# Kernel tuning notes

Hardware: AMD Instinct MI355X
Metric: run time of the kernel (lower is better)

## Reference

```python
import jax, jax.numpy as jnp
import numpy as np

N, F, D, E, L, T = 20000, 512, 256, 200000, 3, 2  # nodes, raw feat, hidden, edges/etype, layers, etypes


def _layernorm(x, g, b, eps=1e-5):
    mu = jnp.mean(x, axis=-1, keepdims=True)
    var = jnp.mean(jnp.square(x - mu), axis=-1, keepdims=True)
    return (x - mu) * jax.lax.rsqrt(var + eps) * g + b


def setup_inputs() -> dict:
    key = jax.random.key(0)
    ks = jax.random.split(key, 12)
    s = 0.02
    return {
        "x": jax.random.normal(ks[0], (N, F), dtype=jnp.float32),
        "src": jax.random.randint(ks[1], (T, E), 0, N, dtype=jnp.int32),
        "dst": jax.random.randint(ks[2], (T, E), 0, N, dtype=jnp.int32),
        # HeteroLinear (single ntype)
        "Wlin": jax.random.normal(ks[3], (D, F), dtype=jnp.float32) * s,
        "blin": jnp.zeros((D,), dtype=jnp.float32),
        # stacked per-layer, per-etype SAGEConv('pool') params
        "Wpool": jax.random.normal(ks[4], (L, T, D, D), dtype=jnp.float32) * s,
        "bpool": jnp.zeros((L, T, D), dtype=jnp.float32),
        "Wself": jax.random.normal(ks[5], (L, T, D, D), dtype=jnp.float32) * s,
        "Wneigh": jax.random.normal(ks[6], (L, T, D, D), dtype=jnp.float32) * s,
        "bconv": jnp.zeros((L, T, D), dtype=jnp.float32),
        "gamma": jnp.ones((L, T, D), dtype=jnp.float32),
        "beta": jnp.zeros((L, T, D), dtype=jnp.float32),
    }


def reference(x, src, dst, Wlin, blin, Wpool, bpool, Wself, Wneigh, bconv, gamma, beta):
    n = x.shape[0]
    # HeteroLinear: raw features -> embed
    h = x @ Wlin.T + blin
    for l in range(L):
        out = None
        for t in range(T):  # per edge-type SAGEConv, aggregator='pool'
            hp = jax.nn.relu(h @ Wpool[l, t].T + bpool[l, t])        # fc_pool + relu on src nodes
            m = hp[src[t]]                                            # gather [E, D]
            neigh = jax.ops.segment_max(m, dst[t], num_segments=n)    # max-pool reduce
            neigh = jnp.where(jnp.isneginf(neigh), 0.0, neigh)        # zero-in-degree -> 0 (DGL)
            rst = h @ Wself[l, t].T + neigh @ Wneigh[l, t].T + bconv[l, t]
            if l < L - 1:
                rst = jax.nn.relu(rst)                                # activation before norm
            rst = _layernorm(rst, gamma[l, t], beta[l, t])
            out = rst if out is None else out + rst                   # HeteroGraphConv 'sum'
        h = out
    return h
```

## Files before the change

kernel.cpp:

```cpp
#include <hip/hip_runtime.h>

#define N_NODES 20000
#define F_IN    512
#define D_H     256
#define E_EDGES 200000
#define L_LAYERS 3
#define T_ETYPES 2

typedef __attribute__((ext_vector_type(8))) short bf16x8;
typedef __attribute__((ext_vector_type(4))) float f32x4;

__device__ __forceinline__ unsigned short f2b(float f) {
    unsigned int u = __float_as_uint(f);
    u = (u + 0x7FFFu + ((u >> 16) & 1u)) >> 16;
    return (unsigned short)u;
}
__device__ __forceinline__ unsigned int pack2(float a, float b) {
    return (unsigned int)f2b(a) | ((unsigned int)f2b(b) << 16);
}

__device__ __forceinline__ void gload16(const unsigned short* g, unsigned short* l)
{
    __builtin_amdgcn_global_load_lds(
        (const __attribute__((address_space(1))) void*)g,
        (__attribute__((address_space(3))) void*)l, 16, 0, 0);
}

__device__ __forceinline__ void shufg8(const float* __restrict__ s,
                                       unsigned short* __restrict__ d,
                                       int NO, int K, int o8)
{
    const int matsz8 = (NO * K) >> 3;
    const int mat = o8 / matsz8;
    const int rem = o8 - mat * matsz8;
    const int dst = rem << 3;
    const int slab = dst >> 12;
    const int w = dst & 4095;
    const int spr = K >> 5;
    const int slab_n = slab / spr, slab_k = slab - slab_n * spr;
    const int nl = (((w >> 9) & 7) << 4) + ((w >> 3) & 15);
    const int kk = ((w >> 7) & 3) << 3;
    const size_t soff = (size_t)mat * NO * K + (size_t)(slab_n * 128 + nl) * K
                      + slab_k * 32 + kk;
    const float4 a = *(const float4*)(s + soff);
    const float4 b = *(const float4*)(s + soff + 4);
    uint4 u;
    u.x = pack2(a.x, a.y); u.y = pack2(a.z, a.w);
    u.z = pack2(b.x, b.y); u.w = pack2(b.z, b.w);
    *(uint4*)(d + (size_t)mat * NO * K + dst) = u;
}

__global__ __launch_bounds__(256) void prep_kernel(
    const float* __restrict__ x,  unsigned short* __restrict__ xb, int nx8,
    const float* __restrict__ s0, unsigned short* __restrict__ d0, int NO0, int K0, int n08,
    const float* __restrict__ s1, unsigned short* __restrict__ d1, int NO1, int K1, int n18,
    const float* __restrict__ s2, unsigned short* __restrict__ d2, int NO2, int K2, int n28,
    const float* __restrict__ s3, unsigned short* __restrict__ d3, int NO3, int K3, int n38)
{
    int i = blockIdx.x * 256 + threadIdx.x;
    if (i < nx8) {
        const float4 a = ((const float4*)x)[i * 2];
        const float4 b = ((const float4*)x)[i * 2 + 1];
        uint4 u;
        u.x = pack2(a.x, a.y); u.y = pack2(a.z, a.w);
        u.z = pack2(b.x, b.y); u.w = pack2(b.z, b.w);
        ((uint4*)xb)[i] = u;
        return;
    }
    i -= nx8;
    if (i < n08) { shufg8(s0, d0, NO0, K0, i); return; }
    if ((i -= n08) < n18) { shufg8(s1, d1, NO1, K1, i); return; }
    if ((i -= n18) < n28) { shufg8(s2, d2, NO2, K2, i); return; }
    if ((i -= n28) < n38) { shufg8(s3, d3, NO3, K3, i); return; }
}

template <int NSTEPS>
__global__ __launch_bounds__(256) void gemm_lds(
    const unsigned short* __restrict__ A,
    const unsigned short* __restrict__ Wf,
    const float* __restrict__ bias, unsigned short* __restrict__ Cout,
    int M, int ldc, int relu)
{
    __shared__ __align__(16) unsigned short As[3][4096];
    __shared__ __align__(16) unsigned short Bs[3][4096];
    const int K = NSTEPS * 32;
    const int tid = threadIdx.x, lane = tid & 63, w = tid >> 6;
    const int wm = w >> 1, wn = w & 1;
    const int bm = blockIdx.y * 128, bn = blockIdx.x * 128;
    const unsigned short* slab0 = Wf + (((size_t)blockIdx.x * NSTEPS) << 12);

    size_t aoff[2];
#pragma unroll
    for (int q = 0; q < 2; ++q) {
        const int c = q * 256 + tid;
        const int mi = c >> 6, ww = c & 63, r = ww & 15, kq = ww >> 4;
        const int rg = min(bm + mi * 16 + r, M - 1);
        aoff[q] = (size_t)rg * K + kq * 8;
    }

    const int cbase = bn + wn * 64 + (lane & 15);
    float bj[4];
#pragma unroll
    for (int j = 0; j < 4; ++j) bj[j] = bias[cbase + j * 16];
    asm volatile("" ::: "memory");

    f32x4 acc[4][4] = {};

#define GL_STAGE(S, BUF) do { \
    _Pragma("unroll") \
    for (int q_ = 0; q_ < 2; ++q_) { \
        gload16(A + aoff[q_] + (S) * 32, &As[BUF][(q_ * 256 + w * 64) * 8]); \
        gload16(slab0 + (((size_t)(S)) << 12) + (size_t)(q_ * 256 + tid) * 8, \
                &Bs[BUF][(q_ * 256 + w * 64) * 8]); \
    } \
} while (0)

    GL_STAGE(0, 0);
    GL_STAGE(1, 1);
#pragma unroll
    for (int s = 0; s < NSTEPS; ++s) {
        if (s + 1 < NSTEPS) asm volatile("s_waitcnt vmcnt(4)" ::: "memory");
        else                asm volatile("s_waitcnt vmcnt(0)" ::: "memory");
        __builtin_amdgcn_s_barrier();
        asm volatile("" ::: "memory");
        if (s + 2 < NSTEPS) GL_STAGE(s + 2, (s + 2) % 3);
        const int buf = s % 3;
        bf16x8 a[4], b[4];
#pragma unroll
        for (int mi = 0; mi < 4; ++mi)
            a[mi] = *(const bf16x8*)((const char*)As[buf] + ((wm * 4 + mi) << 10) + lane * 16);
#pragma unroll
        for (int j = 0; j < 4; ++j)
            b[j] = *(const bf16x8*)((const char*)Bs[buf] + ((wn * 4 + j) << 10) + lane * 16);
#pragma unroll
        for (int mi = 0; mi < 4; ++mi)
#pragma unroll
            for (int j = 0; j < 4; ++j)
                acc[mi][j] = __builtin_amdgcn_mfma_f32_16x16x32_bf16(a[mi], b[j], acc[mi][j], 0, 0, 0);
    }
#undef GL_STAGE

    const int rb = bm + wm * 64 + ((lane >> 4) << 2);
#pragma unroll
    for (int j = 0; j < 4; ++j) {
#pragma unroll
        for (int mi = 0; mi < 4; ++mi)
#pragma unroll
            for (int r = 0; r < 4; ++r) {
                const int row = rb + mi * 16 + r;
                if (row < M) {
                    float v = acc[mi][j][r] + bj[j];
                    if (relu) v = fmaxf(v, 0.f);
                    Cout[(size_t)row * ldc + cbase + j * 16] = f2b(v);
                }
            }
    }
}

template <int RELU>
__global__ __launch_bounds__(256) void tail_gemm(
    const unsigned short* __restrict__ h,
    const unsigned short* __restrict__ neigh,
    const unsigned short* __restrict__ Ws,
    const unsigned short* __restrict__ Wn,
    const float* __restrict__ bias,
    float* __restrict__ R)
{
    __shared__ __align__(16) unsigned short As[3][4096];
    __shared__ __align__(16) unsigned short Bs[3][4096];
    const int tid = threadIdx.x, lane = tid & 63, w = tid >> 6;
    const int wm = w >> 1, wn = w & 1;
    const int bm = blockIdx.y * 128;
    const int cs = blockIdx.x;
    const int e  = cs >> 1;
    const unsigned short* Bself  = Ws + (size_t)e * 65536 + (cs & 1) * 32768;
    const unsigned short* Bneigh = Wn + (size_t)e * 65536 + (cs & 1) * 32768;

    size_t aoffH[2], aoffN[2];
#pragma unroll
    for (int q = 0; q < 2; ++q) {
        const int c = q * 256 + tid;
        const int mi = c >> 6, ww = c & 63, r = ww & 15, kq = ww >> 4;
        const int rg = min(bm + mi * 16 + r, N_NODES - 1);
        aoffH[q] = (size_t)rg * 256 + kq * 8;
        aoffN[q] = (size_t)rg * 512 + e * 256 + kq * 8;
    }

    const int cbase = cs * 128 + wn * 64 + (lane & 15);
    float bj[4];
#pragma unroll
    for (int j = 0; j < 4; ++j) bj[j] = bias[cbase + j * 16];
    asm volatile("" ::: "memory");

    f32x4 acc[4][4] = {};

#define TG_STAGE(S, BUF) do { \
    _Pragma("unroll") \
    for (int q_ = 0; q_ < 2; ++q_) { \
        const unsigned short* as_ = ((S) < 8) ? (h + aoffH[q_] + (S) * 32) \
                                              : (neigh + aoffN[q_] + ((S) - 8) * 32); \
        gload16(as_, &As[BUF][(q_ * 256 + w * 64) * 8]); \
        const unsigned short* bs_ = (((S) < 8) ? (Bself + (S) * 4096) \
                                               : (Bneigh + ((S) - 8) * 4096)) \
                                    + (size_t)(q_ * 256 + tid) * 8; \
        gload16(bs_, &Bs[BUF][(q_ * 256 + w * 64) * 8]); \
    } \
} while (0)

    TG_STAGE(0, 0);
    TG_STAGE(1, 1);
#pragma unroll
    for (int s = 0; s < 16; ++s) {
        if (s + 1 < 16) asm volatile("s_waitcnt vmcnt(4)" ::: "memory");
        else            asm volatile("s_waitcnt vmcnt(0)" ::: "memory");
        __builtin_amdgcn_s_barrier();
        asm volatile("" ::: "memory");
        if (s + 2 < 16) TG_STAGE(s + 2, (s + 2) % 3);
        const int buf = s % 3;
        bf16x8 a[4], b[4];
#pragma unroll
        for (int mi = 0; mi < 4; ++mi)
            a[mi] = *(const bf16x8*)((const char*)As[buf] + ((wm * 4 + mi) << 10) + lane * 16);
#pragma unroll
        for (int j = 0; j < 4; ++j)
            b[j] = *(const bf16x8*)((const char*)Bs[buf] + ((wn * 4 + j) << 10) + lane * 16);
#pragma unroll
        for (int mi = 0; mi < 4; ++mi)
#pragma unroll
            for (int j = 0; j < 4; ++j)
                acc[mi][j] = __builtin_amdgcn_mfma_f32_16x16x32_bf16(a[mi], b[j], acc[mi][j], 0, 0, 0);
    }
#undef TG_STAGE

    const int rb = bm + wm * 64 + ((lane >> 4) << 2);
#pragma unroll
    for (int j = 0; j < 4; ++j) {
#pragma unroll
        for (int mi = 0; mi < 4; ++mi)
#pragma unroll
            for (int r = 0; r < 4; ++r) {
                const int row = rb + mi * 16 + r;
                if (row < N_NODES) {
                    float v = acc[mi][j][r] + bj[j];
                    if (RELU) v = fmaxf(v, 0.f);
                    R[(size_t)row * 512 + cbase + j * 16] = v;
                }
            }
    }
}

template <int LAST>
__global__ __launch_bounds__(256) void ln_sum_kernel(
    const float* __restrict__ R,
    const float* __restrict__ gamma,
    const float* __restrict__ beta,
    void* __restrict__ outp)
{
    const int row  = blockIdx.x * 4 + (threadIdx.x >> 6);
    const int lane = threadIdx.x & 63;
    const float4 v0 = ((const float4*)R)[(size_t)row * 128 + lane];
    const float4 v1 = ((const float4*)R)[(size_t)row * 128 + 64 + lane];
    float s0 = v0.x + v0.y + v0.z + v0.w;
    float q0 = v0.x * v0.x + v0.y * v0.y + v0.z * v0.z + v0.w * v0.w;
    float s1 = v1.x + v1.y + v1.z + v1.w;
    float q1 = v1.x * v1.x + v1.y * v1.y + v1.z * v1.z + v1.w * v1.w;
#pragma unroll
    for (int o = 1; o < 64; o <<= 1) {
        s0 += __shfl_xor(s0, o); q0 += __shfl_xor(q0, o);
        s1 += __shfl_xor(s1, o); q1 += __shfl_xor(q1, o);
    }
    const float m0 = s0 * (1.f / 256.f), m1 = s1 * (1.f / 256.f);
    const float i0 = rsqrtf(q0 * (1.f / 256.f) - m0 * m0 + 1e-5f);
    const float i1 = rsqrtf(q1 * (1.f / 256.f) - m1 * m1 + 1e-5f);
    const float4 g0 = ((const float4*)gamma)[lane];
    const float4 b0 = ((const float4*)beta)[lane];
    const float4 g1 = ((const float4*)(gamma + 256))[lane];
    const float4 b1 = ((const float4*)(beta + 256))[lane];
    const float o0 = (v0.x - m0) * i0 * g0.x + b0.x + (v1.x - m1) * i1 * g1.x + b1.x;
    const float o1 = (v0.y - m0) * i0 * g0.y + b0.y + (v1.y - m1) * i1 * g1.y + b1.y;
    const float o2 = (v0.z - m0) * i0 * g0.z + b0.z + (v1.z - m1) * i1 * g1.z + b1.z;
    const float o3 = (v0.w - m0) * i0 * g0.w + b0.w + (v1.w - m1) * i1 * g1.w + b1.w;
    if (LAST) {
        ((float4*)outp)[(size_t)row * 64 + lane] = make_float4(o0, o1, o2, o3);
    } else {
        ushort4 u;
        u.x = f2b(o0); u.y = f2b(o1); u.z = f2b(o2); u.w = f2b(o3);
        ((ushort4*)outp)[(size_t)row * 64 + lane] = u;
    }
}

__global__ __launch_bounds__(256) void count_deg_kernel(
    const int* __restrict__ dst, int* __restrict__ cnt, int E2)
{
    int e = blockIdx.x * 256 + threadIdx.x;
    if (e < E2) {
        const int base = (e >= E_EDGES) ? N_NODES : 0;
        atomicAdd(&cnt[base + dst[e]], 1);
    }
}

__global__ __launch_bounds__(256) void scanA_kernel(
    const int* __restrict__ cnt, int* __restrict__ incl, int* __restrict__ bsum, int n)
{
    __shared__ int tmp[256];
    const int tid = threadIdx.x;
    const int i = blockIdx.x * 256 + tid;
    const int v = (i < n) ? cnt[i] : 0;
    tmp[tid] = v;
    __syncthreads();
#pragma unroll
    for (int o = 1; o < 256; o <<= 1) {
        const int t = (tid >= o) ? tmp[tid - o] : 0;
        __syncthreads();
        tmp[tid] += t;
        __syncthreads();
    }
    if (i < n) incl[i] = tmp[tid];
    if (tid == 255) bsum[blockIdx.x] = tmp[255];
}

__global__ __launch_bounds__(256) void scanB_kernel(int* __restrict__ bsum, int nb)
{
    __shared__ int tmp[256];
    const int tid = threadIdx.x;
    const int v = (tid < nb) ? bsum[tid] : 0;
    tmp[tid] = v;
    __syncthreads();
#pragma unroll
    for (int o = 1; o < 256; o <<= 1) {
        const int t = (tid >= o) ? tmp[tid - o] : 0;
        __syncthreads();
        tmp[tid] += t;
        __syncthreads();
    }
    if (tid < nb) bsum[tid] = tmp[tid] - v;
}

__global__ __launch_bounds__(256) void scanC_kernel(
    const int* __restrict__ cnt, const int* __restrict__ incl,
    const int* __restrict__ bsum, int* __restrict__ off, int* __restrict__ cursor, int n)
{
    const int i = blockIdx.x * 256 + threadIdx.x;
    if (i < n) {
        const int e = incl[i] + bsum[blockIdx.x];
        off[i + 1] = e;
        cursor[i] = e - cnt[i];
    }
    if (i == 0) off[0] = 0;
}

__global__ __launch_bounds__(256) void fill_csr_kernel(
    const int* __restrict__ src, const int* __restrict__ dst,
    int* __restrict__ cursor, int* __restrict__ esrc, int E2)
{
    int e = blockIdx.x * 256 + threadIdx.x;
    if (e < E2) {
        const int base = (e >= E_EDGES) ? N_NODES : 0;
        const int pos = atomicAdd(&cursor[base + dst[e]], 1);
        esrc[pos] = src[e];
    }
}

__device__ __forceinline__ ushort4 umax4(ushort4 a, ushort4 b)
{
    a.x = a.x > b.x ? a.x : b.x;
    a.y = a.y > b.y ? a.y : b.y;
    a.z = a.z > b.z ? a.z : b.z;
    a.w = a.w > b.w ? a.w : b.w;
    return a;
}

__global__ __launch_bounds__(256) void seg_max_kernel(
    const unsigned short* __restrict__ hp, const int* __restrict__ off,
    const int* __restrict__ esrc, unsigned short* __restrict__ neigh)
{
    const int g = blockIdx.x * 4 + (threadIdx.x >> 6);
    if (g >= 2 * N_NODES) return;
    const int t = (g >= N_NODES) ? 1 : 0;
    const int node = g - t * N_NODES;
    const int lane = threadIdx.x & 63;
    const int co = t * D_H + lane * 4;
    const int e0 = off[g], e1 = off[g + 1];
    ushort4 acc = make_ushort4(0, 0, 0, 0);
    int e = e0;
    for (; e + 4 <= e1; e += 4) {
        const int s0 = esrc[e + 0], s1 = esrc[e + 1];
        const int s2 = esrc[e + 2], s3 = esrc[e + 3];
        const ushort4 v0 = *(const ushort4*)(hp + (size_t)s0 * 512 + co);
        const ushort4 v1 = *(const ushort4*)(hp + (size_t)s1 * 512 + co);
        const ushort4 v2 = *(const ushort4*)(hp + (size_t)s2 * 512 + co);
        const ushort4 v3 = *(const ushort4*)(hp + (size_t)s3 * 512 + co);
        acc = umax4(umax4(umax4(acc, v0), umax4(v1, v2)), v3);
    }
    for (; e < e1; ++e)
        acc = umax4(acc, *(const ushort4*)(hp + (size_t)esrc[e] * 512 + co));
    *(ushort4*)(neigh + (size_t)node * 512 + co) = acc;
}

extern "C" void kernel_launch(void* const* d_in, const int* in_sizes, int n_in,
                              void* d_out, int out_size, void* d_ws, size_t ws_size,
                              hipStream_t stream)
{
    const float* x      = (const float*)d_in[0];
    const int*   src    = (const int*)d_in[1];
    const int*   dst    = (const int*)d_in[2];
    const float* Wlin   = (const float*)d_in[3];
    const float* blin   = (const float*)d_in[4];
    const float* Wpool  = (const float*)d_in[5];
    const float* bpool  = (const float*)d_in[6];
    const float* Wself  = (const float*)d_in[7];
    const float* Wneigh = (const float*)d_in[8];
    const float* bconv  = (const float*)d_in[9];
    const float* gamma  = (const float*)d_in[10];
    const float* beta   = (const float*)d_in[11];

    const size_t NB = (size_t)N_NODES * D_H;
    char* p = (char*)d_ws;
    unsigned short* hp_b    = (unsigned short*)p; p += NB * 2 * T_ETYPES;
    unsigned short* neigh_b = (unsigned short*)p; p += NB * 2 * T_ETYPES;
    unsigned short* h_a     = (unsigned short*)p; p += NB * 2;
    unsigned short* h_b     = (unsigned short*)p; p += NB * 2;
    unsigned short* xb      = (unsigned short*)p; p += (size_t)N_NODES * F_IN * 2;
    float*          Rbuf    = (float*)p;          p += (size_t)N_NODES * 512 * 4;
    unsigned short* wlin_f  = (unsigned short*)p; p += (size_t)D_H * F_IN * 2;
    const size_t WSZ = (size_t)L_LAYERS * T_ETYPES * D_H * D_H;
    unsigned short* wpool_f = (unsigned short*)p; p += WSZ * 2;
    unsigned short* wself_f = (unsigned short*)p; p += WSZ * 2;
    unsigned short* wneigh_f= (unsigned short*)p; p += WSZ * 2;
    int* ip = (int*)p;
    const int NT = T_ETYPES * N_NODES;
    int* cnt    = ip; ip += NT;
    int* incl   = ip; ip += NT;
    int* off    = ip; ip += NT + 1;
    int* cursor = ip; ip += NT;
    int* esrc   = ip; ip += T_ETYPES * E_EDGES;
    int* bsum   = ip; ip += 256;

    const dim3 blk(256);
    const int E2 = T_ETYPES * E_EDGES;
    const dim3 e2grid((E2 + 255) / 256);
    const int nScanBlk = (NT + 255) / 256;

    {
        const int nx8  = N_NODES * F_IN / 8;
        const int nl8  = D_H * F_IN / 8;
        const int nw8  = (int)(WSZ / 8);
        const int tot  = nx8 + nl8 + 3 * nw8;
        prep_kernel<<<dim3((tot + 255) / 256), blk, 0, stream>>>(
            x, xb, nx8,
            Wlin, wlin_f, D_H, F_IN, nl8,
            Wpool, wpool_f, T_ETYPES * D_H, D_H, nw8,
            Wself, wself_f, D_H, D_H, nw8,
            Wneigh, wneigh_f, D_H, D_H, nw8);
    }

    hipMemsetAsync(cnt, 0, (size_t)NT * sizeof(int), stream);
    count_deg_kernel<<<e2grid, blk, 0, stream>>>(dst, cnt, E2);
    scanA_kernel<<<dim3(nScanBlk), blk, 0, stream>>>(cnt, incl, bsum, NT);
    scanB_kernel<<<dim3(1), blk, 0, stream>>>(bsum, nScanBlk);
    scanC_kernel<<<dim3(nScanBlk), blk, 0, stream>>>(cnt, incl, bsum, off, cursor, NT);
    fill_csr_kernel<<<e2grid, blk, 0, stream>>>(src, dst, cursor, esrc, E2);

    const int MB = (N_NODES + 127) / 128;

    gemm_lds<16><<<dim3(2, MB), blk, 0, stream>>>(
        xb, wlin_f, blin, h_a, N_NODES, D_H, 0);

    unsigned short* h = h_a;
    unsigned short* hn = h_b;
    const dim3 sgrid((2 * N_NODES + 3) / 4);
    const dim3 lngrid(N_NODES / 4);
    for (int l = 0; l < L_LAYERS; ++l) {
        gemm_lds<8><<<dim3(4, MB), blk, 0, stream>>>(
            h, wpool_f + (size_t)l * T_ETYPES * D_H * D_H,
            bpool + (size_t)l * T_ETYPES * D_H, hp_b, N_NODES, T_ETYPES * D_H, 1);
        seg_max_kernel<<<sgrid, blk, 0, stream>>>(hp_b, off, esrc, neigh_b);
        const size_t wlo = (size_t)l * T_ETYPES * D_H * D_H;
        const size_t blo = (size_t)l * T_ETYPES * D_H;
        if (l < L_LAYERS - 1) {
            tail_gemm<1><<<dim3(4, MB), blk, 0, stream>>>(
                h, neigh_b, wself_f + wlo, wneigh_f + wlo, bconv + blo, Rbuf);
            ln_sum_kernel<0><<<lngrid, blk, 0, stream>>>(
                Rbuf, gamma + blo, beta + blo, hn);
        } else {
            tail_gemm<0><<<dim3(4, MB), blk, 0, stream>>>(
                h, neigh_b, wself_f + wlo, wneigh_f + wlo, bconv + blo, Rbuf);
            ln_sum_kernel<1><<<lngrid, blk, 0, stream>>>(
                Rbuf, gamma + blo, beta + blo, d_out);
        }
        unsigned short* tmp = h; h = hn; hn = tmp;
    }
}
```

Measured before the change: 410.2 us.

## Use 512-thread GEMM blocks with 4x2 wave split and grouped block ordering

Both GEMM kernels move from 256-thread blocks, where each wave computes a 64x64 tile, to 512-thread blocks, where each wave computes a 64x32 tile. Each thread now issues one A and one B async load per stage instead of two, so the vmcnt wait drops from 4 to 2. The 2D grid becomes a 1D grid that walks groups of 8 row-blocks across all column slabs, so neighbouring blocks share the A rows in L2. Accumulators per thread are halved, which may allow more waves in flight, at the cost of more blocks and barriers spanning 8 waves.

```diff
diff --git a/kernel.cpp b/kernel.cpp
--- a/kernel.cpp
+++ b/kernel.cpp
@@ -74,8 +74,8 @@
     if ((i -= n28) < n38) { shufg8(s3, d3, NO3, K3, i); return; }
 }
 
-template <int NSTEPS>
-__global__ __launch_bounds__(256) void gemm_lds(
+template <int NSTEPS, int CS>
+__global__ __launch_bounds__(512) void gemm_lds(
     const unsigned short* __restrict__ A,
     const unsigned short* __restrict__ Wf,
     const float* __restrict__ bias, unsigned short* __restrict__ Cout,
@@ -84,65 +84,61 @@
     __shared__ __align__(16) unsigned short As[3][4096];
     __shared__ __align__(16) unsigned short Bs[3][4096];
     const int K = NSTEPS * 32;
-    const int tid = threadIdx.x, lane = tid & 63, w = tid >> 6;
-    const int wm = w >> 1, wn = w & 1;
-    const int bm = blockIdx.y * 128, bn = blockIdx.x * 128;
-    const unsigned short* slab0 = Wf + (((size_t)blockIdx.x * NSTEPS) << 12);
-
-    size_t aoff[2];
-#pragma unroll
-    for (int q = 0; q < 2; ++q) {
-        const int c = q * 256 + tid;
-        const int mi = c >> 6, ww = c & 63, r = ww & 15, kq = ww >> 4;
-        const int rg = min(bm + mi * 16 + r, M - 1);
-        aoff[q] = (size_t)rg * K + kq * 8;
-    }
-
-    const int cbase = bn + wn * 64 + (lane & 15);
-    float bj[4];
-#pragma unroll
-    for (int j = 0; j < 4; ++j) bj[j] = bias[cbase + j * 16];
+    const int tid = threadIdx.x, lane = tid & 63;
+    const int w = tid >> 6, wm = w >> 2, wn = w & 3;
+    const int id = blockIdx.x;
+    const int g = id / (8 * CS), rem = id - g * (8 * CS);
+    const int cs = rem >> 3, bmi = (g << 3) | (rem & 7);
+    const int MB = (M + 127) >> 7;
+    if (bmi >= MB) return;
+    const int bm = bmi * 128;
+    const unsigned short* slab0 = Wf + (((size_t)cs * NSTEPS) << 12);
+
+    const int rg = min(bm + ((tid >> 6) << 4) + (tid & 15), M - 1);
+    const size_t aoff = (size_t)rg * K + ((tid >> 4) & 3) * 8;
+    const unsigned short* bsrc = slab0 + (size_t)tid * 8;
+
+    const int cbase = cs * 128 + wn * 32 + (lane & 15);
+    float bj[2];
+#pragma unroll
+    for (int j = 0; j < 2; ++j) bj[j] = bias[cbase + j * 16];
     asm volatile("" ::: "memory");
 
-    f32x4 acc[4][4] = {};
+    f32x4 acc[4][2] = {};
 
 #define GL_STAGE(S, BUF) do { \
-    _Pragma("unroll") \
-    for (int q_ = 0; q_ < 2; ++q_) { \
-        gload16(A + aoff[q_] + (S) * 32, &As[BUF][(q_ * 256 + w * 64) * 8]); \
-        gload16(slab0 + (((size_t)(S)) << 12) + (size_t)(q_ * 256 + tid) * 8, \
-                &Bs[BUF][(q_ * 256 + w * 64) * 8]); \
-    } \
+    gload16(A + aoff + (S) * 32, &As[BUF][(size_t)tid * 8]); \
+    gload16(bsrc + (((size_t)(S)) << 12), &Bs[BUF][(size_t)tid * 8]); \
 } while (0)
 
     GL_STAGE(0, 0);
     GL_STAGE(1, 1);
 #pragma unroll
     for (int s = 0; s < NSTEPS; ++s) {
-        if (s + 1 < NSTEPS) asm volatile("s_waitcnt vmcnt(4)" ::: "memory");
+        if (s + 1 < NSTEPS) asm volatile("s_waitcnt vmcnt(2)" ::: "memory");
         else                asm volatile("s_waitcnt vmcnt(0)" ::: "memory");
         __builtin_amdgcn_s_barrier();
         asm volatile("" ::: "memory");
         if (s + 2 < NSTEPS) GL_STAGE(s + 2, (s + 2) % 3);
         const int buf = s % 3;
-        bf16x8 a[4], b[4];
+        bf16x8 a[4], b[2];
 #pragma unroll
         for (int mi = 0; mi < 4; ++mi)
             a[mi] = *(const bf16x8*)((const char*)As[buf] + ((wm * 4 + mi) << 10) + lane * 16);
 #pragma unroll
-        for (int j = 0; j < 4; ++j)
-            b[j] = *(const bf16x8*)((const char*)Bs[buf] + ((wn * 4 + j) << 10) + lane * 16);
-#pragma unroll
-        for (int mi = 0; mi < 4; ++mi)
-#pragma unroll
-            for (int j = 0; j < 4; ++j)
+        for (int j = 0; j < 2; ++j)
+            b[j] = *(const bf16x8*)((const char*)Bs[buf] + ((wn * 2 + j) << 10) + lane * 16);
+#pragma unroll
+        for (int mi = 0; mi < 4; ++mi)
+#pragma unroll
+            for (int j = 0; j < 2; ++j)
                 acc[mi][j] = __builtin_amdgcn_mfma_f32_16x16x32_bf16(a[mi], b[j], acc[mi][j], 0, 0, 0);
     }
 #undef GL_STAGE
 
     const int rb = bm + wm * 64 + ((lane >> 4) << 2);
 #pragma unroll
-    for (int j = 0; j < 4; ++j) {
+    for (int j = 0; j < 2; ++j) {
 #pragma unroll
         for (int mi = 0; mi < 4; ++mi)
 #pragma unroll
@@ -158,7 +154,7 @@
 }
 
 template <int RELU>
-__global__ __launch_bounds__(256) void tail_gemm(
+__global__ __launch_bounds__(512) void tail_gemm(
     const unsigned short* __restrict__ h,
     const unsigned short* __restrict__ neigh,
     const unsigned short* __restrict__ Ws,
@@ -168,73 +164,68 @@
 {
     __shared__ __align__(16) unsigned short As[3][4096];
     __shared__ __align__(16) unsigned short Bs[3][4096];
-    const int tid = threadIdx.x, lane = tid & 63, w = tid >> 6;
-    const int wm = w >> 1, wn = w & 1;
-    const int bm = blockIdx.y * 128;
-    const int cs = blockIdx.x;
+    const int tid = threadIdx.x, lane = tid & 63;
+    const int w = tid >> 6, wm = w >> 2, wn = w & 3;
+    const int id = blockIdx.x;
+    const int g = id >> 5, rem = id & 31;
+    const int cs = rem >> 3, bmi = (g << 3) | (rem & 7);
+    const int MB = (N_NODES + 127) >> 7;
+    if (bmi >= MB) return;
+    const int bm = bmi * 128;
     const int e  = cs >> 1;
     const unsigned short* Bself  = Ws + (size_t)e * 65536 + (cs & 1) * 32768;
     const unsigned short* Bneigh = Wn + (size_t)e * 65536 + (cs & 1) * 32768;
 
-    size_t aoffH[2], aoffN[2];
-#pragma unroll
-    for (int q = 0; q < 2; ++q) {
-        const int c = q * 256 + tid;
-        const int mi = c >> 6, ww = c & 63, r = ww & 15, kq = ww >> 4;
-        const int rg = min(bm + mi * 16 + r, N_NODES - 1);
-        aoffH[q] = (size_t)rg * 256 + kq * 8;
-        aoffN[q] = (size_t)rg * 512 + e * 256 + kq * 8;
-    }
-
-    const int cbase = cs * 128 + wn * 64 + (lane & 15);
-    float bj[4];
-#pragma unroll
-    for (int j = 0; j < 4; ++j) bj[j] = bias[cbase + j * 16];
+    const int rg = min(bm + ((tid >> 6) << 4) + (tid & 15), N_NODES - 1);
+    const size_t aoffH = (size_t)rg * 256 + ((tid >> 4) & 3) * 8;
+    const size_t aoffN = (size_t)rg * 512 + e * 256 + ((tid >> 4) & 3) * 8;
+
+    const int cbase = cs * 128 + wn * 32 + (lane & 15);
+    float bj[2];
+#pragma unroll
+    for (int j = 0; j < 2; ++j) bj[j] = bias[cbase + j * 16];
     asm volatile("" ::: "memory");
 
-    f32x4 acc[4][4] = {};
+    f32x4 acc[4][2] = {};
 
 #define TG_STAGE(S, BUF) do { \
-    _Pragma("unroll") \
-    for (int q_ = 0; q_ < 2; ++q_) { \
-        const unsigned short* as_ = ((S) < 8) ? (h + aoffH[q_] + (S) * 32) \
-                                              : (neigh + aoffN[q_] + ((S) - 8) * 32); \
-        gload16(as_, &As[BUF][(q_ * 256 + w * 64) * 8]); \
-        const unsigned short* bs_ = (((S) < 8) ? (Bself + (S) * 4096) \
-                                               : (Bneigh + ((S) - 8) * 4096)) \
-                                    + (size_t)(q_ * 256 + tid) * 8; \
-        gload16(bs_, &Bs[BUF][(q_ * 256 + w * 64) * 8]); \
-    } \
+    const unsigned short* as_ = ((S) < 8) ? (h + aoffH + (S) * 32) \
+                                          : (neigh + aoffN + ((S) - 8) * 32); \
+    gload16(as_, &As[BUF][(size_t)tid * 8]); \
+    const unsigned short* bs_ = (((S) < 8) ? (Bself + (S) * 4096) \
+                                           : (Bneigh + ((S) - 8) * 4096)) \
+                                + (size_t)tid * 8; \
+    gload16(bs_, &Bs[BUF][(size_t)tid * 8]); \
 } while (0)
 
     TG_STAGE(0, 0);
     TG_STAGE(1, 1);
 #pragma unroll
     for (int s = 0; s < 16; ++s) {
-        if (s + 1 < 16) asm volatile("s_waitcnt vmcnt(4)" ::: "memory");
+        if (s + 1 < 16) asm volatile("s_waitcnt vmcnt(2)" ::: "memory");
         else            asm volatile("s_waitcnt vmcnt(0)" ::: "memory");
         __builtin_amdgcn_s_barrier();
         asm volatile("" ::: "memory");
         if (s + 2 < 16) TG_STAGE(s + 2, (s + 2) % 3);
         const int buf = s % 3;
-        bf16x8 a[4], b[4];
+        bf16x8 a[4], b[2];
 #pragma unroll
         for (int mi = 0; mi < 4; ++mi)
             a[mi] = *(const bf16x8*)((const char*)As[buf] + ((wm * 4 + mi) << 10) + lane * 16);
 #pragma unroll
-        for (int j = 0; j < 4; ++j)
-            b[j] = *(const bf16x8*)((const char*)Bs[buf] + ((wn * 4 + j) << 10) + lane * 16);
-#pragma unroll
-        for (int mi = 0; mi < 4; ++mi)
-#pragma unroll
-            for (int j = 0; j < 4; ++j)
+        for (int j = 0; j < 2; ++j)
+            b[j] = *(const bf16x8*)((const char*)Bs[buf] + ((wn * 2 + j) << 10) + lane * 16);
+#pragma unroll
+        for (int mi = 0; mi < 4; ++mi)
+#pragma unroll
+            for (int j = 0; j < 2; ++j)
                 acc[mi][j] = __builtin_amdgcn_mfma_f32_16x16x32_bf16(a[mi], b[j], acc[mi][j], 0, 0, 0);
     }
 #undef TG_STAGE
 
     const int rb = bm + wm * 64 + ((lane >> 4) << 2);
 #pragma unroll
-    for (int j = 0; j < 4; ++j) {
+    for (int j = 0; j < 2; ++j) {
 #pragma unroll
         for (int mi = 0; mi < 4; ++mi)
 #pragma unroll
@@ -437,6 +428,7 @@
     int* bsum   = ip; ip += 256;
 
     const dim3 blk(256);
+    const dim3 blk512(512);
     const int E2 = T_ETYPES * E_EDGES;
     const dim3 e2grid((E2 + 255) / 256);
     const int nScanBlk = (NT + 255) / 256;
@@ -461,9 +453,9 @@
     scanC_kernel<<<dim3(nScanBlk), blk, 0, stream>>>(cnt, incl, bsum, off, cursor, NT);
     fill_csr_kernel<<<e2grid, blk, 0, stream>>>(src, dst, cursor, esrc, E2);
 
-    const int MB = (N_NODES + 127) / 128;
-
-    gemm_lds<16><<<dim3(2, MB), blk, 0, stream>>>(
+    const int MGRP = ((N_NODES + 127) / 128 + 7) / 8;
+
+    gemm_lds<16, 2><<<dim3(MGRP * 16), blk512, 0, stream>>>(
         xb, wlin_f, blin, h_a, N_NODES, D_H, 0);
 
     unsigned short* h = h_a;
@@ -471,19 +463,19 @@
     const dim3 sgrid((2 * N_NODES + 3) / 4);
     const dim3 lngrid(N_NODES / 4);
     for (int l = 0; l < L_LAYERS; ++l) {
-        gemm_lds<8><<<dim3(4, MB), blk, 0, stream>>>(
+        gemm_lds<8, 4><<<dim3(MGRP * 32), blk512, 0, stream>>>(
             h, wpool_f + (size_t)l * T_ETYPES * D_H * D_H,
             bpool + (size_t)l * T_ETYPES * D_H, hp_b, N_NODES, T_ETYPES * D_H, 1);
         seg_max_kernel<<<sgrid, blk, 0, stream>>>(hp_b, off, esrc, neigh_b);
         const size_t wlo = (size_t)l * T_ETYPES * D_H * D_H;
         const size_t blo = (size_t)l * T_ETYPES * D_H;
         if (l < L_LAYERS - 1) {
-            tail_gemm<1><<<dim3(4, MB), blk, 0, stream>>>(
+            tail_gemm<1><<<dim3(MGRP * 32), blk512, 0, stream>>>(
                 h, neigh_b, wself_f + wlo, wneigh_f + wlo, bconv + blo, Rbuf);
             ln_sum_kernel<0><<<lngrid, blk, 0, stream>>>(
                 Rbuf, gamma + blo, beta + blo, hn);
         } else {
-            tail_gemm<0><<<dim3(4, MB), blk, 0, stream>>>(
+            tail_gemm<0><<<dim3(MGRP * 32), blk512, 0, stream>>>(
                 h, neigh_b, wself_f + wlo, wneigh_f + wlo, bconv + blo, Rbuf);
             ln_sum_kernel<1><<<lngrid, blk, 0, stream>>>(
                 Rbuf, gamma + blo, beta + blo, d_out);
```

Result: faster. 390.6 us (-4.8%).
